# Kernel tuning notes

Hardware: AMD Instinct MI355X
Metric: run time of the kernel (lower is better)

## Reference

```python
import jax, jax.numpy as jnp
import numpy as np

D_MODEL, D_K, D_V, H = 1024, 64, 64, 16
B, N = 4, 2048


def setup_inputs() -> dict:
    key = jax.random.key(0)
    ks = jax.random.split(key, 11)
    s = 0.02
    return {
        "Q": jax.random.normal(ks[0], (B, N, D_MODEL), jnp.float32),
        "K": jax.random.normal(ks[1], (B, N, D_MODEL), jnp.float32),
        "V": jax.random.normal(ks[2], (B, N, D_MODEL), jnp.float32),
        # stacked per-head projection weights: [h, d_model, d_k]
        "Wq": jax.random.normal(ks[3], (H, D_MODEL, D_K), jnp.float32) * s,
        "bq": jax.random.normal(ks[4], (H, D_K), jnp.float32) * s,
        "Wk": jax.random.normal(ks[5], (H, D_MODEL, D_K), jnp.float32) * s,
        "bk": jax.random.normal(ks[6], (H, D_K), jnp.float32) * s,
        "Wv": jax.random.normal(ks[7], (H, D_MODEL, D_V), jnp.float32) * s,
        "bv": jax.random.normal(ks[8], (H, D_V), jnp.float32) * s,
        "Wo": jax.random.normal(ks[9], (H * D_V, D_MODEL), jnp.float32) * s,
        "bo": jax.random.normal(ks[10], (D_MODEL,), jnp.float32) * s,
        "apply_mask": 1,
    }


def reference(Q, K, V, Wq, bq, Wk, bk, Wv, bv, Wo, bo, apply_mask):
    # fused per-head projections: [b, h, n, d_k]
    q = jnp.einsum("bnd,hdk->bhnk", Q, Wq) + bq[None, :, None, :]
    k = jnp.einsum("bnd,hdk->bhnk", K, Wk) + bk[None, :, None, :]
    v = jnp.einsum("bnd,hdv->bhnv", V, Wv) + bv[None, :, None, :]
    scores = jnp.einsum("bhnk,bhmk->bhnm", q, k) / jnp.sqrt(
        jnp.asarray(D_K, q.dtype)
    )
    if apply_mask:
        n = Q.shape[1]
        causal = jnp.tril(jnp.ones((n, n), dtype=bool))
        scores = jnp.where(causal[None, None], scores, -jnp.inf)
    weights = jax.nn.softmax(scores, axis=-1)
    out = jnp.einsum("bhnm,bhmv->bhnv", weights, v)
    # concat heads: [b, n, h*d_v]
    out = out.transpose(0, 2, 1, 3).reshape(Q.shape[0], Q.shape[1], H * D_V)
    return out @ Wo + bo
```

## Files before the change

kernel.cpp:

```cpp
#include <hip/hip_runtime.h>
#include <hip/hip_bf16.h>

#define H 16
#define DM 1024
#define DK 64
#define B_ 4
#define N_ 2048

typedef __attribute__((ext_vector_type(8))) short bf16x8;
typedef __attribute__((ext_vector_type(4))) short s16x4;
typedef __attribute__((ext_vector_type(4))) float f32x4;

static __device__ __forceinline__ short f2bs(float x) {
    __hip_bfloat16 b = __float2bfloat16(x);
    return *reinterpret_cast<short*>(&b);
}

static __device__ __forceinline__ void async16(const void* g, void* l) {
    __builtin_amdgcn_global_load_lds(
        (const __attribute__((address_space(1))) void*)g,
        (__attribute__((address_space(3))) void*)l, 16, 0, 0);
}

__global__ __launch_bounds__(256) void transpose_weights(
    const float* __restrict__ Wq, const float* __restrict__ Wk,
    const float* __restrict__ Wv, const float* __restrict__ Wo,
    short* __restrict__ wqT, short* __restrict__ wkT,
    short* __restrict__ wvT, short* __restrict__ woT)
{
    __shared__ float tile[64][65];
    int z = blockIdx.y;
    int t = threadIdx.x;
    int tj = t & 63, ti = t >> 6;

    if (z < 3) {
        const float* src = (z == 0) ? Wq : (z == 1) ? Wk : Wv;
        short* dst = (z == 0) ? wqT : (z == 1) ? wkT : wvT;
        int h = blockIdx.x >> 4;
        int dmt = blockIdx.x & 15;
        #pragma unroll
        for (int r = 0; r < 16; ++r) {
            int i = r * 4 + ti;
            tile[i][tj] = src[((size_t)h * 1024 + dmt * 64 + i) * 64 + tj];
        }
        __syncthreads();
        #pragma unroll
        for (int r = 0; r < 16; ++r) {
            int dk = r * 4 + ti;
            dst[((size_t)h * 64 + dk) * 1024 + dmt * 64 + tj] = f2bs(tile[tj][dk]);
        }
    } else {
        int kt = blockIdx.x >> 4;
        int nt = blockIdx.x & 15;
        #pragma unroll
        for (int r = 0; r < 16; ++r) {
            int i = r * 4 + ti;
            tile[i][tj] = Wo[((size_t)kt * 64 + i) * 1024 + nt * 64 + tj];
        }
        __syncthreads();
        #pragma unroll
        for (int r = 0; r < 16; ++r) {
            int jn = r * 4 + ti;
            woT[((size_t)nt * 64 + jn) * 1024 + kt * 64 + tj] = f2bs(tile[tj][jn]);
        }
    }
}

__global__ __launch_bounds__(256) void convert_bf16(
    const float* __restrict__ Q, const float* __restrict__ K, const float* __restrict__ V,
    short* __restrict__ Qb, short* __restrict__ Kb, short* __restrict__ Vb)
{
    int which = blockIdx.y;
    const float* s = (which == 0) ? Q : (which == 1) ? K : V;
    short* d = (which == 0) ? Qb : (which == 1) ? Kb : Vb;
    size_t i = ((size_t)blockIdx.x * 256 + threadIdx.x) * 8;
    f32x4 a = *(const f32x4*)(s + i);
    f32x4 b = *(const f32x4*)(s + i + 4);
    bf16x8 p;
    #pragma unroll
    for (int j = 0; j < 4; ++j) { p[j] = f2bs(a[j]); p[4 + j] = f2bs(b[j]); }
    *(bf16x8*)(d + i) = p;
}

static __device__ __forceinline__ void gemm_stage(
    const char* Ab, const char* Bb, size_t kb, char* As, char* Bs, int lane, int w)
{
    int r0 = w * 32 + (lane >> 2);
    int g  = ((lane & 3) ^ ((lane >> 3) & 3)) << 4;
    int dst0 = w * 2048 + lane * 16;
    async16(Ab + (size_t)r0 * 2048 + kb + g, As + dst0);
    async16(Ab + (size_t)(r0 + 16) * 2048 + kb + g, As + dst0 + 1024);
    async16(Bb + (size_t)r0 * 2048 + kb + g, Bs + dst0);
    async16(Bb + (size_t)(r0 + 16) * 2048 + kb + g, Bs + dst0 + 1024);
}

static __device__ __forceinline__ void gemm_mainloop(
    const short* __restrict__ A, const short* __restrict__ BT,
    int rowM0, int colN0, char* As, char* Bs, f32x4 (&acc)[4][4])
{
    int tid = threadIdx.x;
    int lane = tid & 63, w = tid >> 6;
    int l16 = lane & 15, quad = lane >> 4;
    int wm = w >> 1, wn = w & 1;
    int xg = (quad ^ ((l16 >> 1) & 3)) << 4;

    const char* Ab = (const char*)A + (size_t)rowM0 * 2048;
    const char* Bb = (const char*)BT + (size_t)colN0 * 2048;

    gemm_stage(Ab, Bb, 0, As, Bs, lane, w);
    for (int it = 0; it < 32; ++it) {
        __syncthreads();
        int cur = (it & 1) * 8192;
        if (it + 1 < 32) {
            int nxt = ((it + 1) & 1) * 8192;
            gemm_stage(Ab, Bb, (size_t)(it + 1) * 64, As + nxt, Bs + nxt, lane, w);
        }
        bf16x8 a[4], b[4];
        #pragma unroll
        for (int i = 0; i < 4; ++i)
            a[i] = *(const bf16x8*)(As + cur + (wm * 64 + i * 16 + l16) * 64 + xg);
        #pragma unroll
        for (int j = 0; j < 4; ++j)
            b[j] = *(const bf16x8*)(Bs + cur + (wn * 64 + j * 16 + l16) * 64 + xg);
        #pragma unroll
        for (int i = 0; i < 4; ++i)
            #pragma unroll
            for (int j = 0; j < 4; ++j)
                acc[i][j] = __builtin_amdgcn_mfma_f32_16x16x32_bf16(a[i], b[j], acc[i][j], 0, 0, 0);
    }
}

__global__ __launch_bounds__(256) void proj_gemm(
    const short* __restrict__ Qb, const short* __restrict__ Kb, const short* __restrict__ Vb,
    const short* __restrict__ wqT, const short* __restrict__ wkT, const short* __restrict__ wvT,
    const float* __restrict__ bq, const float* __restrict__ bk, const float* __restrict__ bv,
    short* __restrict__ qbuf, short* __restrict__ kbuf, short* __restrict__ vTbuf)
{
    __shared__ char As[16384], Bs[16384];
    int which = blockIdx.z;
    const short* A  = (which == 0) ? Qb : (which == 1) ? Kb : Vb;
    const short* BT = (which == 0) ? wqT : (which == 1) ? wkT : wvT;
    const float* bias = (which == 0) ? bq : (which == 1) ? bk : bv;

    int rowM0 = blockIdx.x * 128;
    int colN0 = blockIdx.y * 128;

    f32x4 acc[4][4];
    #pragma unroll
    for (int i = 0; i < 4; ++i)
        #pragma unroll
        for (int j = 0; j < 4; ++j) acc[i][j] = (f32x4){0.f, 0.f, 0.f, 0.f};

    gemm_mainloop(A, BT, rowM0, colN0, As, Bs, acc);

    int lane = threadIdx.x & 63, w = threadIdx.x >> 6;
    int l16 = lane & 15, quad = lane >> 4;
    int wm = w >> 1, wn = w & 1;

    if (which == 2) {
        #pragma unroll
        for (int j = 0; j < 4; ++j) {
            int col = colN0 + wn * 64 + j * 16 + l16;
            int hh = col >> 6, dv = col & 63;
            float bs = bias[col];
            #pragma unroll
            for (int i = 0; i < 4; ++i) {
                int rowb = rowM0 + wm * 64 + i * 16 + quad * 4;
                int bb = rowb >> 11, n0 = rowb & 2047;
                s16x4 pk;
                #pragma unroll
                for (int r = 0; r < 4; ++r) pk[r] = f2bs(acc[i][j][r] + bs);
                *(s16x4*)(vTbuf + (((size_t)bb * H + hh) * DK + dv) * N_ + n0) = pk;
            }
        }
    } else {
        short* dst = (which == 0) ? qbuf : kbuf;
        float scl = (which == 0) ? 0.180336880f : 1.0f;
        #pragma unroll
        for (int j = 0; j < 4; ++j) {
            int col = colN0 + wn * 64 + j * 16 + l16;
            float bs = bias[col];
            #pragma unroll
            for (int i = 0; i < 4; ++i) {
                int rowb = rowM0 + wm * 64 + i * 16 + quad * 4;
                #pragma unroll
                for (int r = 0; r < 4; ++r)
                    dst[(size_t)(rowb + r) * 1024 + col] = f2bs((acc[i][j][r] + bs) * scl);
            }
        }
    }
}

__global__ __launch_bounds__(256) void out_gemm(
    const short* __restrict__ obuf, const short* __restrict__ woT,
    const float* __restrict__ bo, float* __restrict__ out)
{
    __shared__ char As[16384], Bs[16384];
    int rowM0 = blockIdx.x * 128;
    int colN0 = blockIdx.y * 128;

    f32x4 acc[4][4];
    #pragma unroll
    for (int i = 0; i < 4; ++i)
        #pragma unroll
        for (int j = 0; j < 4; ++j) acc[i][j] = (f32x4){0.f, 0.f, 0.f, 0.f};

    gemm_mainloop(obuf, woT, rowM0, colN0, As, Bs, acc);

    int lane = threadIdx.x & 63, w = threadIdx.x >> 6;
    int l16 = lane & 15, quad = lane >> 4;
    int wm = w >> 1, wn = w & 1;

    #pragma unroll
    for (int j = 0; j < 4; ++j) {
        int col = colN0 + wn * 64 + j * 16 + l16;
        float bs = bo[col];
        #pragma unroll
        for (int i = 0; i < 4; ++i) {
            int rowb = rowM0 + wm * 64 + i * 16 + quad * 4;
            #pragma unroll
            for (int r = 0; r < 4; ++r)
                out[(size_t)(rowb + r) * 1024 + col] = acc[i][j][r] + bs;
        }
    }
}

__global__ __launch_bounds__(256) void flash_kernel(
    const short* __restrict__ qbuf, const short* __restrict__ kbuf, const short* __restrict__ vT,
    short* __restrict__ obuf, const int* __restrict__ amask)
{
    __shared__ short Ks[4096];
    __shared__ short Vs[4096];
    __shared__ short plds[4][16][72];

    int tid = threadIdx.x;
    int lane = tid & 63, wave = tid >> 6;
    int l16 = lane & 15, quad = lane >> 4;
    int bh = blockIdx.y;
    int b = bh >> 4, h = bh & 15;
    int msk = amask[0];

    int i8 = lane >> 3, i7 = lane & 7;
    int sg = (i7 ^ i8) << 4;
    int skey = wave * 16 + i8;
    char* kdst0 = (char*)Ks + wave * 2048 + lane * 16;
    char* vdst0 = (char*)Vs + wave * 2048 + lane * 16;

    const char* kbase = (const char*)(kbuf + (size_t)b * 2048 * 1024 + h * 64);
    const char* vbase = (const char*)(vT + ((size_t)(b * 16 + h) * 64) * 2048);

    int xr = l16 & 7;
    int g0 = (quad ^ xr) << 4;
    int g1 = ((4 | quad) ^ xr) << 4;

    for (int pass = 0; pass < 2; ++pass) {
        int qt = pass ? (31 - (int)blockIdx.x) : (int)blockIdx.x;
        int qb0 = qt * 64;
        int qw = qb0 + wave * 16;
        int nkb = msk ? (qt + 1) : 32;

        const short* qp = qbuf + ((size_t)(b * 2048 + qw + l16)) * 1024 + h * 64;
        bf16x8 aq0 = *(const bf16x8*)(qp + quad * 8);
        bf16x8 aq1 = *(const bf16x8*)(qp + 32 + quad * 8);

        f32x4 o[4];
        float lsum[4];
        #pragma unroll
        for (int i = 0; i < 4; ++i) { o[i] = (f32x4){0.f, 0.f, 0.f, 0.f}; lsum[i] = 0.f; }

        for (int ib = 0; ib < nkb; ++ib) {
            int kb = ib * 64;
            async16(kbase + (size_t)(kb + skey) * 2048 + sg, kdst0);
            async16(kbase + (size_t)(kb + skey + 8) * 2048 + sg, kdst0 + 1024);
            async16(vbase + (size_t)skey * 4096 + kb * 2 + sg, vdst0);
            async16(vbase + (size_t)(skey + 8) * 4096 + kb * 2 + sg, vdst0 + 1024);
            __syncthreads();

            f32x4 s[4];
            #pragma unroll
            for (int nt = 0; nt < 4; ++nt) {
                const char* kr = (const char*)Ks + (nt * 16 + l16) * 128;
                bf16x8 b0 = *(const bf16x8*)(kr + g0);
                bf16x8 b1 = *(const bf16x8*)(kr + g1);
                f32x4 t = (f32x4){0.f, 0.f, 0.f, 0.f};
                t = __builtin_amdgcn_mfma_f32_16x16x32_bf16(aq0, b0, t, 0, 0, 0);
                t = __builtin_amdgcn_mfma_f32_16x16x32_bf16(aq1, b1, t, 0, 0, 0);
                s[nt] = t;
            }

            if (msk && (kb + 63 > qw)) {
                #pragma unroll
                for (int r = 0; r < 4; ++r) {
                    int row = qw + quad * 4 + r;
                    #pragma unroll
                    for (int nt = 0; nt < 4; ++nt) {
                        int col = kb + nt * 16 + l16;
                        if (col > row) s[nt][r] = -3e38f;
                    }
                }
            }

            #pragma unroll
            for (int r = 0; r < 4; ++r) {
                float p0 = exp2f(s[0][r]), p1 = exp2f(s[1][r]);
                float p2 = exp2f(s[2][r]), p3 = exp2f(s[3][r]);
                s[0][r] = p0; s[1][r] = p1; s[2][r] = p2; s[3][r] = p3;
                lsum[r] += (p0 + p1) + (p2 + p3);
            }

            __builtin_amdgcn_wave_barrier();
            #pragma unroll
            for (int r = 0; r < 4; ++r)
                #pragma unroll
                for (int nt = 0; nt < 4; ++nt)
                    plds[wave][quad * 4 + r][nt * 16 + l16] = f2bs(s[nt][r]);
            __builtin_amdgcn_wave_barrier();
            bf16x8 ap0 = *(const bf16x8*)(&plds[wave][l16][quad * 8]);
            bf16x8 ap1 = *(const bf16x8*)(&plds[wave][l16][32 + quad * 8]);
            __builtin_amdgcn_wave_barrier();

            #pragma unroll
            for (int vb = 0; vb < 4; ++vb) {
                const char* vr = (const char*)Vs + (vb * 16 + l16) * 128;
                bf16x8 v0 = *(const bf16x8*)(vr + g0);
                bf16x8 v1 = *(const bf16x8*)(vr + g1);
                o[vb] = __builtin_amdgcn_mfma_f32_16x16x32_bf16(ap0, v0, o[vb], 0, 0, 0);
                o[vb] = __builtin_amdgcn_mfma_f32_16x16x32_bf16(ap1, v1, o[vb], 0, 0, 0);
            }
            __syncthreads();
        }

        #pragma unroll
        for (int r = 0; r < 4; ++r) {
            float t = lsum[r];
            #pragma unroll
            for (int off = 1; off < 16; off <<= 1) t += __shfl_xor(t, off, 64);
            float inv = 1.0f / t;
            int row = qw + quad * 4 + r;
            #pragma unroll
            for (int vb = 0; vb < 4; ++vb)
                obuf[((size_t)(b * 2048 + row)) * 1024 + h * 64 + vb * 16 + l16] =
                    f2bs(o[vb][r] * inv);
        }
    }
}

extern "C" void kernel_launch(void* const* d_in, const int* in_sizes, int n_in,
                              void* d_out, int out_size, void* d_ws, size_t ws_size,
                              hipStream_t stream)
{
    const float* Q  = (const float*)d_in[0];
    const float* K  = (const float*)d_in[1];
    const float* V  = (const float*)d_in[2];
    const float* Wq = (const float*)d_in[3];
    const float* bq = (const float*)d_in[4];
    const float* Wk = (const float*)d_in[5];
    const float* bk = (const float*)d_in[6];
    const float* Wv = (const float*)d_in[7];
    const float* bv = (const float*)d_in[8];
    const float* Wo = (const float*)d_in[9];
    const float* bo = (const float*)d_in[10];
    const int* amask = (const int*)d_in[11];
    float* out = (float*)d_out;

    char* ws = (char*)d_ws;
    const size_t SZ = (size_t)B_ * N_ * DM * sizeof(short);
    const size_t SZW = (size_t)H * DK * DM * sizeof(short);
    short* Qb    = (short*)ws; ws += SZ;
    short* Kb    = (short*)ws; ws += SZ;
    short* Vb    = (short*)ws; ws += SZ;
    short* qbuf  = (short*)ws; ws += SZ;
    short* kbuf  = (short*)ws; ws += SZ;
    short* vTbuf = (short*)ws; ws += SZ;
    short* wqT   = (short*)ws; ws += SZW;
    short* wkT   = (short*)ws; ws += SZW;
    short* wvT   = (short*)ws; ws += SZW;
    short* woT   = (short*)ws; ws += SZW;
    short* obuf  = Qb;

    transpose_weights<<<dim3(256, 4), dim3(256), 0, stream>>>(Wq, Wk, Wv, Wo, wqT, wkT, wvT, woT);
    convert_bf16<<<dim3(4096, 3), dim3(256), 0, stream>>>(Q, K, V, Qb, Kb, Vb);
    proj_gemm<<<dim3(64, 8, 3), dim3(256), 0, stream>>>(Qb, Kb, Vb, wqT, wkT, wvT,
                                                        bq, bk, bv, qbuf, kbuf, vTbuf);
    flash_kernel<<<dim3(16, 64), dim3(256), 0, stream>>>(qbuf, kbuf, vTbuf, obuf, amask);
    out_gemm<<<dim3(64, 8), dim3(256), 0, stream>>>(obuf, woT, bo, out);
}
```

Baseline: 371.3 us.

## Double-buffer flash K/V tiles, merge prep kernels, remap grid, swizzle P staging

The flash kernel now double-buffers K and V tiles in LDS, issuing async loads for the next key block before computing the current one, so there is one barrier per iteration instead of two. It remaps the grid to 1D with grouping across batch-heads for better L2 locality. It also permutes key rows within a tile so the probability matrix can be written to LDS as packed 4-element stores into a swizzled layout. Separately, the weight transpose and input conversion kernels are merged into one launch. These changes add LDS usage and index complexity, and the permuted key mapping must stay consistent with the causal mask.

```diff
diff --git a/kernel.cpp b/kernel.cpp
--- a/kernel.cpp
+++ b/kernel.cpp
@@ -22,22 +22,39 @@
         (__attribute__((address_space(3))) void*)l, 16, 0, 0);
 }
 
-__global__ __launch_bounds__(256) void transpose_weights(
+__global__ __launch_bounds__(256) void prep_kernel(
+    const float* __restrict__ Q, const float* __restrict__ K, const float* __restrict__ V,
     const float* __restrict__ Wq, const float* __restrict__ Wk,
     const float* __restrict__ Wv, const float* __restrict__ Wo,
+    short* __restrict__ Qb, short* __restrict__ Kb, short* __restrict__ Vb,
     short* __restrict__ wqT, short* __restrict__ wkT,
     short* __restrict__ wvT, short* __restrict__ woT)
 {
+    int y = blockIdx.y;
+    if (y < 3) {
+        const float* s = (y == 0) ? Q : (y == 1) ? K : V;
+        short* d = (y == 0) ? Qb : (y == 1) ? Kb : Vb;
+        size_t i = ((size_t)blockIdx.x * 256 + threadIdx.x) * 8;
+        f32x4 a = *(const f32x4*)(s + i);
+        f32x4 b = *(const f32x4*)(s + i + 4);
+        bf16x8 p;
+        #pragma unroll
+        for (int j = 0; j < 4; ++j) { p[j] = f2bs(a[j]); p[4 + j] = f2bs(b[j]); }
+        *(bf16x8*)(d + i) = p;
+        return;
+    }
+    if (blockIdx.x >= 1024) return;
     __shared__ float tile[64][65];
-    int z = blockIdx.y;
+    int z = blockIdx.x >> 8;
+    int bx = blockIdx.x & 255;
     int t = threadIdx.x;
     int tj = t & 63, ti = t >> 6;
 
     if (z < 3) {
         const float* src = (z == 0) ? Wq : (z == 1) ? Wk : Wv;
         short* dst = (z == 0) ? wqT : (z == 1) ? wkT : wvT;
-        int h = blockIdx.x >> 4;
-        int dmt = blockIdx.x & 15;
+        int h = bx >> 4;
+        int dmt = bx & 15;
         #pragma unroll
         for (int r = 0; r < 16; ++r) {
             int i = r * 4 + ti;
@@ -50,8 +67,8 @@
             dst[((size_t)h * 64 + dk) * 1024 + dmt * 64 + tj] = f2bs(tile[tj][dk]);
         }
     } else {
-        int kt = blockIdx.x >> 4;
-        int nt = blockIdx.x & 15;
+        int kt = bx >> 4;
+        int nt = bx & 15;
         #pragma unroll
         for (int r = 0; r < 16; ++r) {
             int i = r * 4 + ti;
@@ -64,22 +81,6 @@
             woT[((size_t)nt * 64 + jn) * 1024 + kt * 64 + tj] = f2bs(tile[tj][jn]);
         }
     }
-}
-
-__global__ __launch_bounds__(256) void convert_bf16(
-    const float* __restrict__ Q, const float* __restrict__ K, const float* __restrict__ V,
-    short* __restrict__ Qb, short* __restrict__ Kb, short* __restrict__ Vb)
-{
-    int which = blockIdx.y;
-    const float* s = (which == 0) ? Q : (which == 1) ? K : V;
-    short* d = (which == 0) ? Qb : (which == 1) ? Kb : Vb;
-    size_t i = ((size_t)blockIdx.x * 256 + threadIdx.x) * 8;
-    f32x4 a = *(const f32x4*)(s + i);
-    f32x4 b = *(const f32x4*)(s + i + 4);
-    bf16x8 p;
-    #pragma unroll
-    for (int j = 0; j < 4; ++j) { p[j] = f2bs(a[j]); p[4 + j] = f2bs(b[j]); }
-    *(bf16x8*)(d + i) = p;
 }
 
 static __device__ __forceinline__ void gemm_stage(
@@ -229,34 +230,41 @@
     const short* __restrict__ qbuf, const short* __restrict__ kbuf, const short* __restrict__ vT,
     short* __restrict__ obuf, const int* __restrict__ amask)
 {
-    __shared__ short Ks[4096];
-    __shared__ short Vs[4096];
-    __shared__ short plds[4][16][72];
+    __shared__ short Ks[2][4096];
+    __shared__ short Vs[2][4096];
+    __shared__ char  plds[4][2048];
+
+    int bid = blockIdx.x;
+    int g = bid & 7, idx = bid >> 3;
+    int bh = g * 8 + (idx >> 4);
+    int xq = idx & 15;
+    int b = bh >> 4, h = bh & 15;
 
     int tid = threadIdx.x;
     int lane = tid & 63, wave = tid >> 6;
     int l16 = lane & 15, quad = lane >> 4;
-    int bh = blockIdx.y;
-    int b = bh >> 4, h = bh & 15;
     int msk = amask[0];
 
     int i8 = lane >> 3, i7 = lane & 7;
     int sg = (i7 ^ i8) << 4;
+    int pk0 = i8 * 4 + wave;
     int skey = wave * 16 + i8;
-    char* kdst0 = (char*)Ks + wave * 2048 + lane * 16;
-    char* vdst0 = (char*)Vs + wave * 2048 + lane * 16;
+    int ldst = wave * 2048 + lane * 16;
 
     const char* kbase = (const char*)(kbuf + (size_t)b * 2048 * 1024 + h * 64);
     const char* vbase = (const char*)(vT + ((size_t)(b * 16 + h) * 64) * 2048);
 
-    int xr = l16 & 7;
-    int g0 = (quad ^ xr) << 4;
-    int g1 = ((4 | quad) ^ xr) << 4;
+    int m7 = l16 & 7;
+    int g0 = (quad ^ m7) << 4;
+    int g1 = ((4 | quad) ^ m7) << 4;
+
+    char* pw = plds[wave];
+    int prd0 = l16 * 128 + g0;
+    int prd1 = l16 * 128 + g1;
 
     for (int pass = 0; pass < 2; ++pass) {
-        int qt = pass ? (31 - (int)blockIdx.x) : (int)blockIdx.x;
-        int qb0 = qt * 64;
-        int qw = qb0 + wave * 16;
+        int qt = pass ? (31 - xq) : xq;
+        int qw = qt * 64 + wave * 16;
         int nkb = msk ? (qt + 1) : 32;
 
         const short* qp = qbuf + ((size_t)(b * 2048 + qw + l16)) * 1024 + h * 64;
@@ -268,18 +276,28 @@
         #pragma unroll
         for (int i = 0; i < 4; ++i) { o[i] = (f32x4){0.f, 0.f, 0.f, 0.f}; lsum[i] = 0.f; }
 
+        async16(kbase + (size_t)pk0 * 2048 + sg, (char*)Ks[0] + ldst);
+        async16(kbase + (size_t)(pk0 + 32) * 2048 + sg, (char*)Ks[0] + ldst + 1024);
+        async16(vbase + (size_t)skey * 4096 + sg, (char*)Vs[0] + ldst);
+        async16(vbase + (size_t)(skey + 8) * 4096 + sg, (char*)Vs[0] + ldst + 1024);
+
         for (int ib = 0; ib < nkb; ++ib) {
+            __syncthreads();
+            int cur = ib & 1;
+            if (ib + 1 < nkb) {
+                int nb = (ib + 1) & 1;
+                size_t kb2 = (size_t)(ib + 1) * 64;
+                async16(kbase + (kb2 + pk0) * 2048 + sg, (char*)Ks[nb] + ldst);
+                async16(kbase + (kb2 + pk0 + 32) * 2048 + sg, (char*)Ks[nb] + ldst + 1024);
+                async16(vbase + (size_t)skey * 4096 + kb2 * 2 + sg, (char*)Vs[nb] + ldst);
+                async16(vbase + (size_t)(skey + 8) * 4096 + kb2 * 2 + sg, (char*)Vs[nb] + ldst + 1024);
+            }
             int kb = ib * 64;
-            async16(kbase + (size_t)(kb + skey) * 2048 + sg, kdst0);
-            async16(kbase + (size_t)(kb + skey + 8) * 2048 + sg, kdst0 + 1024);
-            async16(vbase + (size_t)skey * 4096 + kb * 2 + sg, vdst0);
-            async16(vbase + (size_t)(skey + 8) * 4096 + kb * 2 + sg, vdst0 + 1024);
-            __syncthreads();
 
             f32x4 s[4];
             #pragma unroll
             for (int nt = 0; nt < 4; ++nt) {
-                const char* kr = (const char*)Ks + (nt * 16 + l16) * 128;
+                const char* kr = (const char*)Ks[cur] + (nt * 16 + l16) * 128;
                 bf16x8 b0 = *(const bf16x8*)(kr + g0);
                 bf16x8 b1 = *(const bf16x8*)(kr + g1);
                 f32x4 t = (f32x4){0.f, 0.f, 0.f, 0.f};
@@ -294,7 +312,7 @@
                     int row = qw + quad * 4 + r;
                     #pragma unroll
                     for (int nt = 0; nt < 4; ++nt) {
-                        int col = kb + nt * 16 + l16;
+                        int col = kb + l16 * 4 + nt;
                         if (col > row) s[nt][r] = -3e38f;
                     }
                 }
@@ -310,24 +328,26 @@
 
             __builtin_amdgcn_wave_barrier();
             #pragma unroll
-            for (int r = 0; r < 4; ++r)
-                #pragma unroll
-                for (int nt = 0; nt < 4; ++nt)
-                    plds[wave][quad * 4 + r][nt * 16 + l16] = f2bs(s[nt][r]);
+            for (int r = 0; r < 4; ++r) {
+                int row = quad * 4 + r;
+                s16x4 pk;
+                pk[0] = f2bs(s[0][r]); pk[1] = f2bs(s[1][r]);
+                pk[2] = f2bs(s[2][r]); pk[3] = f2bs(s[3][r]);
+                *(s16x4*)(pw + row * 128 + (((l16 >> 1) ^ (row & 7)) << 4) + ((l16 & 1) << 3)) = pk;
+            }
             __builtin_amdgcn_wave_barrier();
-            bf16x8 ap0 = *(const bf16x8*)(&plds[wave][l16][quad * 8]);
-            bf16x8 ap1 = *(const bf16x8*)(&plds[wave][l16][32 + quad * 8]);
+            bf16x8 ap0 = *(const bf16x8*)(pw + prd0);
+            bf16x8 ap1 = *(const bf16x8*)(pw + prd1);
             __builtin_amdgcn_wave_barrier();
 
             #pragma unroll
             for (int vb = 0; vb < 4; ++vb) {
-                const char* vr = (const char*)Vs + (vb * 16 + l16) * 128;
+                const char* vr = (const char*)Vs[cur] + (vb * 16 + l16) * 128;
                 bf16x8 v0 = *(const bf16x8*)(vr + g0);
                 bf16x8 v1 = *(const bf16x8*)(vr + g1);
                 o[vb] = __builtin_amdgcn_mfma_f32_16x16x32_bf16(ap0, v0, o[vb], 0, 0, 0);
                 o[vb] = __builtin_amdgcn_mfma_f32_16x16x32_bf16(ap1, v1, o[vb], 0, 0, 0);
             }
-            __syncthreads();
         }
 
         #pragma unroll
@@ -342,6 +362,7 @@
                 obuf[((size_t)(b * 2048 + row)) * 1024 + h * 64 + vb * 16 + l16] =
                     f2bs(o[vb][r] * inv);
         }
+        __syncthreads();
     }
 }
 
@@ -378,10 +399,10 @@
     short* woT   = (short*)ws; ws += SZW;
     short* obuf  = Qb;
 
-    transpose_weights<<<dim3(256, 4), dim3(256), 0, stream>>>(Wq, Wk, Wv, Wo, wqT, wkT, wvT, woT);
-    convert_bf16<<<dim3(4096, 3), dim3(256), 0, stream>>>(Q, K, V, Qb, Kb, Vb);
+    prep_kernel<<<dim3(4096, 4), dim3(256), 0, stream>>>(Q, K, V, Wq, Wk, Wv, Wo,
+                                                         Qb, Kb, Vb, wqT, wkT, wvT, woT);
     proj_gemm<<<dim3(64, 8, 3), dim3(256), 0, stream>>>(Qb, Kb, Vb, wqT, wkT, wvT,
                                                         bq, bk, bv, qbuf, kbuf, vTbuf);
-    flash_kernel<<<dim3(16, 64), dim3(256), 0, stream>>>(qbuf, kbuf, vTbuf, obuf, amask);
+    flash_kernel<<<dim3(1024), dim3(256), 0, stream>>>(qbuf, kbuf, vTbuf, obuf, amask);
     out_gemm<<<dim3(64, 8), dim3(256), 0, stream>>>(obuf, woT, bo, out);
 }
```

New measurement: 358.1 us. -3.5%, faster.
